# Performance work log

Measured on AMD Instinct MI355X. Metric: run time of the kernel, lower is better.

## Reference

```python
import jax, jax.numpy as jnp
import numpy as np

B, T = 128, 2048
O, E, L = 128, 512, 34  # o_size, embed_dim, num_letter


def setup_inputs() -> dict:
    key = jax.random.key(0)
    ks = jax.random.split(key, 16)
    u = lambda k, shape, s: jax.random.uniform(k, shape, jnp.float32, -s, s)
    hk = jax.random.normal(ks[0], (B, T, O), jnp.float32)
    hv = jax.random.normal(ks[1], (B, T, O), jnp.float32)
    y_1 = jax.random.normal(ks[2], (B, E), jnp.float32)
    c_1 = jax.random.normal(ks[3], (B, O), jnp.float32)
    sh_1 = jax.random.normal(ks[4], (B, O), jnp.float32)
    sc_1 = jax.random.normal(ks[5], (B, O), jnp.float32)
    # valid-length mask (each row has at least T//2 valid positions)
    lengths = jax.random.randint(ks[6], (B,), T // 2, T + 1)
    mask = (jnp.arange(T)[None, :] < lengths[:, None]).astype(jnp.float32)
    s_rnn = 1.0 / np.sqrt(O)
    W_ih = u(ks[7], (4 * O, O + E), s_rnn)
    b_ih = u(ks[8], (4 * O,), s_rnn)
    W_hh = u(ks[9], (4 * O, O), s_rnn)
    b_hh = u(ks[10], (4 * O,), s_rnn)
    s1 = 1.0 / np.sqrt(O)
    W1 = u(ks[11], (L, O), s1); b1 = u(ks[12], (L,), s1)
    W2 = u(ks[13], (L, O), s1); b2 = u(ks[14], (L,), s1)
    s3 = 1.0 / np.sqrt(L)
    W3 = u(ks[15], (L, L), s3); b3 = u(jax.random.fold_in(key, 99), (L,), s3)
    return {"hk": hk, "hv": hv, "y_1": y_1, "c_1": c_1, "sh_1": sh_1,
            "sc_1": sc_1, "mask": mask, "W_ih": W_ih, "b_ih": b_ih,
            "W_hh": W_hh, "b_hh": b_hh, "W1": W1, "b1": b1,
            "W2": W2, "b2": b2, "W3": W3, "b3": b3}


def reference(hk, hv, y_1, c_1, sh_1, sc_1, mask,
              W_ih, b_ih, W_hh, b_hh, W1, b1, W2, b2, W3, b3):
    # LSTMCell (PyTorch gate order: i, f, g, o)
    x = jnp.concatenate([y_1, c_1], axis=1)            # [B, O+E]
    gates = x @ W_ih.T + b_ih + sh_1 @ W_hh.T + b_hh   # [B, 4O]
    i, f, g, o = jnp.split(gates, 4, axis=1)
    sc = jax.nn.sigmoid(f) * sc_1 + jax.nn.sigmoid(i) * jnp.tanh(g)
    sh = jax.nn.sigmoid(o) * jnp.tanh(sc)
    # attention scores keyed on cell state sc (faithful to source)
    scores = jnp.einsum('bto,bo->bt', hk, sc)          # [B, T]
    attn = jax.nn.softmax(scores, axis=1) * mask
    attn = attn / jnp.sum(attn, axis=1, keepdims=True)
    c = jnp.einsum('bt,bto->bo', attn, hv)             # [B, O]
    out = jax.nn.relu(sh @ W1.T + b1 + c @ W2.T + b2)
    out = jax.nn.softmax(out @ W3.T + b3, axis=1)      # [B, L]
    return (out, c, sh, sc)
```

## Files before the change

### kernel.cpp

```cpp
#include <hip/hip_runtime.h>
#include <math.h>

#define BB 128
#define TT 2048
#define OO 128
#define EE 512
#define LL 34
#define XDIM 640
#define CHUNKS 16
#define CHUNK_LEN 128

__device__ __forceinline__ float sigmoidf_(float x) { return 1.0f / (1.0f + __expf(-x)); }

__global__ __launch_bounds__(256) void lstm_kernel(
    const float* __restrict__ y1, const float* __restrict__ c1,
    const float* __restrict__ sh1, const float* __restrict__ sc1,
    const float* __restrict__ Wih, const float* __restrict__ bih,
    const float* __restrict__ Whh, const float* __restrict__ bhh,
    float* __restrict__ out_sh, float* __restrict__ out_sc)
{
    __shared__ float xs[4][768];
    __shared__ float gbuf[4][4][16];
    const int tid = threadIdx.x;
    const int otile = blockIdx.x;
    const int qb = blockIdx.y * 4;

    for (int idx = tid; idx < 4 * 768; idx += 256) {
        int bi = idx / 768, k = idx - bi * 768;
        int b = qb + bi;
        float v;
        if (k < 512)      v = y1[b * EE + k];
        else if (k < 640) v = c1[b * OO + (k - 512)];
        else              v = sh1[b * OO + (k - 640)];
        xs[bi][k] = v;
    }
    __syncthreads();

    const int g = tid >> 6, l = tid & 63;
    #pragma unroll 2
    for (int i = 0; i < 16; ++i) {
        const int row = g * 128 + otile * 16 + i;
        const float* wr = Wih + (size_t)row * XDIM;
        float a0 = 0.f, a1 = 0.f, a2 = 0.f, a3 = 0.f;
        #pragma unroll
        for (int j = 0; j < 10; ++j) {
            float wv = wr[l + 64 * j];
            a0 += wv * xs[0][l + 64 * j];
            a1 += wv * xs[1][l + 64 * j];
            a2 += wv * xs[2][l + 64 * j];
            a3 += wv * xs[3][l + 64 * j];
        }
        const float* wh = Whh + (size_t)row * OO;
        #pragma unroll
        for (int j = 0; j < 2; ++j) {
            float wv = wh[l + 64 * j];
            a0 += wv * xs[0][640 + l + 64 * j];
            a1 += wv * xs[1][640 + l + 64 * j];
            a2 += wv * xs[2][640 + l + 64 * j];
            a3 += wv * xs[3][640 + l + 64 * j];
        }
        #pragma unroll
        for (int off = 32; off >= 1; off >>= 1) {
            a0 += __shfl_xor(a0, off);
            a1 += __shfl_xor(a1, off);
            a2 += __shfl_xor(a2, off);
            a3 += __shfl_xor(a3, off);
        }
        if (l == 0) {
            float bb = bih[row] + bhh[row];
            gbuf[g][0][i] = a0 + bb;
            gbuf[g][1][i] = a1 + bb;
            gbuf[g][2][i] = a2 + bb;
            gbuf[g][3][i] = a3 + bb;
        }
    }
    __syncthreads();

    if (tid < 64) {
        const int bi = tid >> 4, ol = tid & 15;
        const int b = qb + bi, o = otile * 16 + ol;
        float gi = gbuf[0][bi][ol], gf = gbuf[1][bi][ol];
        float gg = gbuf[2][bi][ol], go = gbuf[3][bi][ol];
        float sc = sigmoidf_(gf) * sc1[b * OO + o] + sigmoidf_(gi) * tanhf(gg);
        float sh = sigmoidf_(go) * tanhf(sc);
        out_sc[b * OO + o] = sc;
        out_sh[b * OO + o] = sh;
    }
}

__global__ __launch_bounds__(256) void attn_kernel(
    const float* __restrict__ hk, const float* __restrict__ hv,
    const float* __restrict__ mask, const float* __restrict__ sc,
    float* __restrict__ ws_c, float2* __restrict__ pbuf)
{
    const int b = blockIdx.y, chunk = blockIdx.x;
    const int tid = threadIdx.x;
    const int sg = tid >> 4, l = tid & 15;
    const int o4 = tid & 31, rr = tid >> 5;

    __shared__ float sm[16], ssum[16];
    __shared__ float wsh[CHUNK_LEN];
    __shared__ float pacc[8][128];

    const float4 scA = *(const float4*)(sc + b * OO + l * 8);
    const float4 scB = *(const float4*)(sc + b * OO + l * 8 + 4);

    const int r0 = chunk * CHUNK_LEN + sg * 8;
    const float* mrow = mask + (size_t)b * TT + r0;
    const float* krow = hk + ((size_t)b * TT + r0) * OO;

    bool val[8];
    #pragma unroll
    for (int i = 0; i < 8; ++i) val[i] = (mrow[i] != 0.f);

    float s[8];
    #pragma unroll
    for (int i = 0; i < 8; ++i) {
        float4 a  = make_float4(0.f, 0.f, 0.f, 0.f);
        float4 c2 = make_float4(0.f, 0.f, 0.f, 0.f);
        if (val[i]) {
            a  = *(const float4*)(krow + (size_t)i * OO + l * 8);
            c2 = *(const float4*)(krow + (size_t)i * OO + l * 8 + 4);
        }
        s[i] = a.x * scA.x + a.y * scA.y + a.z * scA.z + a.w * scA.w
             + c2.x * scB.x + c2.y * scB.y + c2.z * scB.z + c2.w * scB.w;
    }

    const float* mrowB = mask + (size_t)b * TT + chunk * CHUNK_LEN;
    const float* vbase = hv + ((size_t)b * TT + chunk * CHUNK_LEN) * OO + o4 * 4;
    float4 hvb[16];
    #pragma unroll
    for (int j = 0; j < 16; ++j) {
        const int r = rr + 8 * j;
        hvb[j] = make_float4(0.f, 0.f, 0.f, 0.f);
        if (mrowB[r] != 0.f)
            hvb[j] = *(const float4*)(vbase + (size_t)r * OO);
    }

    #pragma unroll
    for (int i = 0; i < 8; ++i) {
        s[i] += __shfl_xor(s[i], 8);
        s[i] += __shfl_xor(s[i], 4);
        s[i] += __shfl_xor(s[i], 2);
        s[i] += __shfl_xor(s[i], 1);
    }
    float msg = -INFINITY;
    #pragma unroll
    for (int i = 0; i < 8; ++i) if (val[i]) msg = fmaxf(msg, s[i]);

    if (l == 0) sm[sg] = msg;
    __syncthreads();
    float mc = sm[0];
    #pragma unroll
    for (int i = 1; i < 16; ++i) mc = fmaxf(mc, sm[i]);

    float psum = 0.f;
    float e[8];
    #pragma unroll
    for (int i = 0; i < 8; ++i) {
        e[i] = val[i] ? __expf(s[i] - mc) : 0.f;
        psum += e[i];
    }
    #pragma unroll
    for (int i = 0; i < 8; ++i)
        if (l == i) wsh[sg * 8 + i] = e[i];
    if (l == 0) ssum[sg] = psum;
    __syncthreads();

    if (tid == 0) {
        float S = 0.f;
        #pragma unroll
        for (int i = 0; i < 16; ++i) S += ssum[i];
        pbuf[(size_t)b * CHUNKS + chunk] = make_float2(mc, S);
    }

    float4 acc = make_float4(0.f, 0.f, 0.f, 0.f);
    #pragma unroll
    for (int j = 0; j < 16; ++j) {
        const float w = wsh[rr + 8 * j];
        acc.x += w * hvb[j].x;
        acc.y += w * hvb[j].y;
        acc.z += w * hvb[j].z;
        acc.w += w * hvb[j].w;
    }
    *(float4*)&pacc[rr][o4 * 4] = acc;
    __syncthreads();

    if (tid < 128) {
        float t = 0.f;
        #pragma unroll
        for (int i = 0; i < 8; ++i) t += pacc[i][tid];
        ws_c[((size_t)b * CHUNKS + chunk) * OO + tid] = t;
    }
}

__global__ __launch_bounds__(256) void final_kernel(
    const float* __restrict__ ws_c, const float2* __restrict__ pbuf,
    const float* __restrict__ sh_in,
    const float* __restrict__ W1, const float* __restrict__ b1,
    const float* __restrict__ W2, const float* __restrict__ b2,
    const float* __restrict__ W3, const float* __restrict__ b3,
    float* __restrict__ out_p, float* __restrict__ out_c)
{
    const int b = blockIdx.x, tid = threadIdx.x;
    __shared__ float marr[CHUNKS], Sarr[CHUNKS], fac[CHUNKS];
    __shared__ float cbuf[128], shbuf[128], h1[LL], zz[LL], red2[2];

    if (tid < CHUNKS) {
        float2 p = pbuf[(size_t)b * CHUNKS + tid];
        marr[tid] = p.x;
        Sarr[tid] = p.y;
    }
    __syncthreads();
    if (tid < CHUNKS) {
        float M = marr[0];
        #pragma unroll
        for (int i = 1; i < CHUNKS; ++i) M = fmaxf(M, marr[i]);
        float S = 0.f;
        #pragma unroll
        for (int i = 0; i < CHUNKS; ++i) S += Sarr[i] * __expf(marr[i] - M);
        fac[tid] = __expf(marr[tid] - M) / S;
    }
    __syncthreads();

    if (tid < 128) {
        float s = 0.f;
        const float* base = ws_c + (size_t)b * CHUNKS * OO + tid;
        #pragma unroll
        for (int i = 0; i < CHUNKS; ++i) s += fac[i] * base[i * OO];
        cbuf[tid] = s;
        out_c[b * OO + tid] = s;
        shbuf[tid] = sh_in[b * OO + tid];
    }
    __syncthreads();

    const int o = tid >> 2, l2 = tid & 3;
    if (o < LL) {
        float a = 0.f;
        const float* w1r = W1 + o * OO;
        const float* w2r = W2 + o * OO;
        #pragma unroll 8
        for (int j = 0; j < 32; ++j) {
            int k = l2 + 4 * j;
            a += w1r[k] * shbuf[k] + w2r[k] * cbuf[k];
        }
        a += __shfl_xor(a, 1);
        a += __shfl_xor(a, 2);
        if (l2 == 0) h1[o] = fmaxf(a + b1[o] + b2[o], 0.f);
    }
    __syncthreads();

    if (o < LL) {
        float z = 0.f;
        const float* w3r = W3 + o * LL;
        for (int j = 0; j < 9; ++j) {
            int k = l2 + 4 * j;
            if (k < LL) z += w3r[k] * h1[k];
        }
        z += __shfl_xor(z, 1);
        z += __shfl_xor(z, 2);
        if (l2 == 0) zz[o] = z + b3[o];
    }
    __syncthreads();
    if (tid == 0) {
        float mm = zz[0];
        for (int i = 1; i < LL; i++) mm = fmaxf(mm, zz[i]);
        float ss = 0.f;
        for (int i = 0; i < LL; i++) ss += __expf(zz[i] - mm);
        red2[0] = mm; red2[1] = ss;
    }
    __syncthreads();
    if (tid < LL) out_p[b * LL + tid] = __expf(zz[tid] - red2[0]) / red2[1];
}

extern "C" void kernel_launch(void* const* d_in, const int* in_sizes, int n_in,
                              void* d_out, int out_size, void* d_ws, size_t ws_size,
                              hipStream_t stream) {
    (void)in_sizes; (void)n_in; (void)out_size; (void)ws_size;
    const float* hk   = (const float*)d_in[0];
    const float* hv   = (const float*)d_in[1];
    const float* y1   = (const float*)d_in[2];
    const float* c1   = (const float*)d_in[3];
    const float* sh1  = (const float*)d_in[4];
    const float* sc1  = (const float*)d_in[5];
    const float* mask = (const float*)d_in[6];
    const float* Wih  = (const float*)d_in[7];
    const float* bih  = (const float*)d_in[8];
    const float* Whh  = (const float*)d_in[9];
    const float* bhh  = (const float*)d_in[10];
    const float* W1   = (const float*)d_in[11];
    const float* b1   = (const float*)d_in[12];
    const float* W2   = (const float*)d_in[13];
    const float* b2   = (const float*)d_in[14];
    const float* W3   = (const float*)d_in[15];
    const float* b3   = (const float*)d_in[16];

    float* out    = (float*)d_out;
    float* out_c  = out + BB * LL;
    float* out_sh = out_c + BB * OO;
    float* out_sc = out_sh + BB * OO;

    float*  ws_c = (float*)d_ws;
    float2* pbuf = (float2*)(ws_c + (size_t)BB * CHUNKS * OO);

    lstm_kernel<<<dim3(8, 32), 256, 0, stream>>>(y1, c1, sh1, sc1, Wih, bih, Whh, bhh,
                                                 out_sh, out_sc);
    attn_kernel<<<dim3(CHUNKS, BB), 256, 0, stream>>>(hk, hv, mask, out_sc, ws_c, pbuf);
    final_kernel<<<BB, 256, 0, stream>>>(ws_c, pbuf, out_sh, W1, b1, W2, b2, W3, b3,
                                         out, out_c);
}
```

Measured before the change: 327.1 us.

## Split attention into per-wave 32-row subchunks with shuffle-only reductions

The attention kernel now gives each wavefront an independent 32-row subchunk. The block-wide max, sum and weighted-V reductions that went through shared memory and __syncthreads are replaced by wave shuffles, and the 16-register hv prefetch buffer is removed. hv is loaded after the softmax and is skipped only when the whole subchunk is masked, while hk rows are now loaded even when masked. The number of partials per batch row rises from 16 to 64, which grows the workspace and the merge work in the final kernel.

```diff
diff --git a/kernel.cpp b/kernel.cpp
--- a/kernel.cpp
+++ b/kernel.cpp
@@ -7,8 +7,8 @@
 #define EE 512
 #define LL 34
 #define XDIM 640
-#define CHUNKS 16
-#define CHUNK_LEN 128
+#define SUBCH 64
+#define SUB_LEN 32
 
 __device__ __forceinline__ float sigmoidf_(float x) { return 1.0f / (1.0f + __expf(-x)); }
 
@@ -93,50 +93,28 @@
     const float* __restrict__ mask, const float* __restrict__ sc,
     float* __restrict__ ws_c, float2* __restrict__ pbuf)
 {
-    const int b = blockIdx.y, chunk = blockIdx.x;
+    const int b = blockIdx.y;
     const int tid = threadIdx.x;
-    const int sg = tid >> 4, l = tid & 15;
-    const int o4 = tid & 31, rr = tid >> 5;
-
-    __shared__ float sm[16], ssum[16];
-    __shared__ float wsh[CHUNK_LEN];
-    __shared__ float pacc[8][128];
+    const int wave = tid >> 6, lane = tid & 63;
+    const int subchunk = blockIdx.x * 4 + wave;
+    const int sg = (lane >> 4) & 3, l = lane & 15;
+    const int r0 = subchunk * SUB_LEN;
 
     const float4 scA = *(const float4*)(sc + b * OO + l * 8);
     const float4 scB = *(const float4*)(sc + b * OO + l * 8 + 4);
-
-    const int r0 = chunk * CHUNK_LEN + sg * 8;
-    const float* mrow = mask + (size_t)b * TT + r0;
-    const float* krow = hk + ((size_t)b * TT + r0) * OO;
-
+    const float* krow = hk + ((size_t)b * TT + r0 + sg * 8) * OO;
+    const float* mrow = mask + (size_t)b * TT + r0 + sg * 8;
+
+    float s[8];
     bool val[8];
     #pragma unroll
-    for (int i = 0; i < 8; ++i) val[i] = (mrow[i] != 0.f);
-
-    float s[8];
-    #pragma unroll
     for (int i = 0; i < 8; ++i) {
-        float4 a  = make_float4(0.f, 0.f, 0.f, 0.f);
-        float4 c2 = make_float4(0.f, 0.f, 0.f, 0.f);
-        if (val[i]) {
-            a  = *(const float4*)(krow + (size_t)i * OO + l * 8);
-            c2 = *(const float4*)(krow + (size_t)i * OO + l * 8 + 4);
-        }
+        val[i] = (mrow[i] != 0.f);
+        float4 a  = *(const float4*)(krow + (size_t)i * OO + l * 8);
+        float4 c2 = *(const float4*)(krow + (size_t)i * OO + l * 8 + 4);
         s[i] = a.x * scA.x + a.y * scA.y + a.z * scA.z + a.w * scA.w
              + c2.x * scB.x + c2.y * scB.y + c2.z * scB.z + c2.w * scB.w;
     }
-
-    const float* mrowB = mask + (size_t)b * TT + chunk * CHUNK_LEN;
-    const float* vbase = hv + ((size_t)b * TT + chunk * CHUNK_LEN) * OO + o4 * 4;
-    float4 hvb[16];
-    #pragma unroll
-    for (int j = 0; j < 16; ++j) {
-        const int r = rr + 8 * j;
-        hvb[j] = make_float4(0.f, 0.f, 0.f, 0.f);
-        if (mrowB[r] != 0.f)
-            hvb[j] = *(const float4*)(vbase + (size_t)r * OO);
-    }
-
     #pragma unroll
     for (int i = 0; i < 8; ++i) {
         s[i] += __shfl_xor(s[i], 8);
@@ -144,54 +122,51 @@
         s[i] += __shfl_xor(s[i], 2);
         s[i] += __shfl_xor(s[i], 1);
     }
-    float msg = -INFINITY;
-    #pragma unroll
-    for (int i = 0; i < 8; ++i) if (val[i]) msg = fmaxf(msg, s[i]);
-
-    if (l == 0) sm[sg] = msg;
-    __syncthreads();
-    float mc = sm[0];
-    #pragma unroll
-    for (int i = 1; i < 16; ++i) mc = fmaxf(mc, sm[i]);
-
-    float psum = 0.f;
+    float m = -INFINITY;
+    #pragma unroll
+    for (int i = 0; i < 8; ++i) if (val[i]) m = fmaxf(m, s[i]);
+    m = fmaxf(m, __shfl_xor(m, 16));
+    m = fmaxf(m, __shfl_xor(m, 32));
+
     float e[8];
+    float ps = 0.f;
     #pragma unroll
     for (int i = 0; i < 8; ++i) {
-        e[i] = val[i] ? __expf(s[i] - mc) : 0.f;
-        psum += e[i];
-    }
-    #pragma unroll
-    for (int i = 0; i < 8; ++i)
-        if (l == i) wsh[sg * 8 + i] = e[i];
-    if (l == 0) ssum[sg] = psum;
-    __syncthreads();
-
-    if (tid == 0) {
-        float S = 0.f;
-        #pragma unroll
-        for (int i = 0; i < 16; ++i) S += ssum[i];
-        pbuf[(size_t)b * CHUNKS + chunk] = make_float2(mc, S);
-    }
-
+        e[i] = val[i] ? __expf(s[i] - m) : 0.f;
+        ps += e[i];
+    }
+    ps += __shfl_xor(ps, 16);
+    ps += __shfl_xor(ps, 32);
+    if (lane == 0)
+        pbuf[(size_t)b * SUBCH + subchunk] = make_float2(m, ps);
+
+    const int c4 = (lane & 31) * 4, rp = lane >> 5;
     float4 acc = make_float4(0.f, 0.f, 0.f, 0.f);
-    #pragma unroll
-    for (int j = 0; j < 16; ++j) {
-        const float w = wsh[rr + 8 * j];
-        acc.x += w * hvb[j].x;
-        acc.y += w * hvb[j].y;
-        acc.z += w * hvb[j].z;
-        acc.w += w * hvb[j].w;
-    }
-    *(float4*)&pacc[rr][o4 * 4] = acc;
-    __syncthreads();
-
-    if (tid < 128) {
-        float t = 0.f;
-        #pragma unroll
-        for (int i = 0; i < 8; ++i) t += pacc[i][tid];
-        ws_c[((size_t)b * CHUNKS + chunk) * OO + tid] = t;
-    }
+    if (ps > 0.f) {
+        const float* vbase = hv + ((size_t)b * TT + r0) * OO + c4;
+        #pragma unroll
+        for (int sgi = 0; sgi < 4; ++sgi) {
+            float wv[8];
+            #pragma unroll
+            for (int i = 0; i < 8; ++i) wv[i] = __shfl(e[i], sgi * 16);
+            #pragma unroll
+            for (int j = 0; j < 4; ++j) {
+                const int row = sgi * 8 + j * 2 + rp;
+                float4 v = *(const float4*)(vbase + (size_t)row * OO);
+                float w = (rp == 0) ? wv[2 * j] : wv[2 * j + 1];
+                acc.x += w * v.x;
+                acc.y += w * v.y;
+                acc.z += w * v.z;
+                acc.w += w * v.w;
+            }
+        }
+    }
+    acc.x += __shfl_xor(acc.x, 32);
+    acc.y += __shfl_xor(acc.y, 32);
+    acc.z += __shfl_xor(acc.z, 32);
+    acc.w += __shfl_xor(acc.w, 32);
+    if (rp == 0)
+        *(float4*)(ws_c + ((size_t)b * SUBCH + subchunk) * OO + c4) = acc;
 }
 
 __global__ __launch_bounds__(256) void final_kernel(
@@ -203,31 +178,31 @@
     float* __restrict__ out_p, float* __restrict__ out_c)
 {
     const int b = blockIdx.x, tid = threadIdx.x;
-    __shared__ float marr[CHUNKS], Sarr[CHUNKS], fac[CHUNKS];
+    __shared__ float marr[SUBCH], Sarr[SUBCH], fac[SUBCH];
     __shared__ float cbuf[128], shbuf[128], h1[LL], zz[LL], red2[2];
 
-    if (tid < CHUNKS) {
-        float2 p = pbuf[(size_t)b * CHUNKS + tid];
+    if (tid < SUBCH) {
+        float2 p = pbuf[(size_t)b * SUBCH + tid];
         marr[tid] = p.x;
         Sarr[tid] = p.y;
     }
     __syncthreads();
-    if (tid < CHUNKS) {
+    if (tid < SUBCH) {
         float M = marr[0];
         #pragma unroll
-        for (int i = 1; i < CHUNKS; ++i) M = fmaxf(M, marr[i]);
+        for (int i = 1; i < SUBCH; ++i) M = fmaxf(M, marr[i]);
         float S = 0.f;
         #pragma unroll
-        for (int i = 0; i < CHUNKS; ++i) S += Sarr[i] * __expf(marr[i] - M);
+        for (int i = 0; i < SUBCH; ++i) S += Sarr[i] * __expf(marr[i] - M);
         fac[tid] = __expf(marr[tid] - M) / S;
     }
     __syncthreads();
 
     if (tid < 128) {
         float s = 0.f;
-        const float* base = ws_c + (size_t)b * CHUNKS * OO + tid;
-        #pragma unroll
-        for (int i = 0; i < CHUNKS; ++i) s += fac[i] * base[i * OO];
+        const float* base = ws_c + (size_t)b * SUBCH * OO + tid;
+        #pragma unroll 8
+        for (int i = 0; i < SUBCH; ++i) s += fac[i] * base[i * OO];
         cbuf[tid] = s;
         out_c[b * OO + tid] = s;
         shbuf[tid] = sh_in[b * OO + tid];
@@ -301,11 +276,11 @@
     float* out_sc = out_sh + BB * OO;
 
     float*  ws_c = (float*)d_ws;
-    float2* pbuf = (float2*)(ws_c + (size_t)BB * CHUNKS * OO);
+    float2* pbuf = (float2*)(ws_c + (size_t)BB * SUBCH * OO);
 
     lstm_kernel<<<dim3(8, 32), 256, 0, stream>>>(y1, c1, sh1, sc1, Wih, bih, Whh, bhh,
                                                  out_sh, out_sc);
-    attn_kernel<<<dim3(CHUNKS, BB), 256, 0, stream>>>(hk, hv, mask, out_sc, ws_c, pbuf);
+    attn_kernel<<<dim3(SUBCH / 4, BB), 256, 0, stream>>>(hk, hv, mask, out_sc, ws_c, pbuf);
     final_kernel<<<BB, 256, 0, stream>>>(ws_c, pbuf, out_sh, W1, b1, W2, b2, W3, b3,
                                          out, out_c);
 }
```

New measurement: 330.6 us. About the same (+1.1%).
